# Performance work log

Measured on AMD Instinct MI355X. Metric: run time of the kernel, lower is better.

The kernel has to match this reference:

```python
import jax, jax.numpy as jnp
import numpy as np
from jax import lax

B, N, K, NCP = 4, 2048, 20, 400
EPS = 1e-5


def _bn(x, gamma, beta, axes):
    # training-mode batch norm (biased variance), channel axis = 1
    m = jnp.mean(x, axis=axes, keepdims=True)
    v = jnp.var(x, axis=axes, keepdims=True)
    shape = [1] * x.ndim
    shape[1] = -1
    return (x - m) * lax.rsqrt(v + EPS) * gamma.reshape(shape) + beta.reshape(shape)


def _knn_idx(x, k):
    # x: [B, C, N] -> idx [B, N, k] (nearest, includes self like torch.cdist+topk(largest=False))
    x2 = jnp.sum(x * x, axis=1)  # [B, N]
    d = x2[:, :, None] + x2[:, None, :] - 2.0 * jnp.einsum('bcn,bcm->bnm', x, x)
    return lax.top_k(-d, k)[1]


def _edge_conv(x, w, gamma, beta, k):
    # x: [B, C, N], w: [O, 2C] -> [B, O, N] (1x1 conv + BN + LeakyReLU + max over k)
    idx = _knn_idx(x, k)                      # [B, N, k]
    xt = jnp.transpose(x, (0, 2, 1))          # [B, N, C]
    b = jnp.arange(xt.shape[0])[:, None, None]
    nbr = xt[b, idx]                          # [B, N, k, C]
    ctr = xt[:, :, None, :]
    feat = jnp.concatenate([nbr - ctr, jnp.broadcast_to(ctr, nbr.shape)], axis=-1)  # [B, N, k, 2C]
    y = jnp.einsum('bnkc,oc->bonk', feat, w)  # [B, O, N, k]
    y = jax.nn.leaky_relu(_bn(y, gamma, beta, axes=(0, 2, 3)), 0.2)
    return jnp.max(y, axis=-1)                # [B, O, N]


def setup_inputs() -> dict:
    key = jax.random.key(0)
    ks = jax.random.split(key, 16)
    rnd = lambda k_, s: jax.random.normal(k_, s, dtype=jnp.float32) * 0.02
    inp = {
        'x': jax.random.normal(ks[0], (B, 3, N), dtype=jnp.float32),
        'w1': rnd(ks[1], (64, 6)),    'g1': jnp.ones(64),   'b1': jnp.zeros(64),
        'w2': rnd(ks[2], (128, 128)), 'g2': jnp.ones(128),  'b2': jnp.zeros(128),
        'w3': rnd(ks[3], (256, 256)), 'g3': jnp.ones(256),  'b3': jnp.zeros(256),
        'w4': rnd(ks[4], (512, 512)), 'g4': jnp.ones(512),  'b4': jnp.zeros(512),
        'w5': rnd(ks[5], (2048, 963)), 'g5': jnp.ones(2048), 'b5': jnp.zeros(2048),
        'w6': rnd(ks[6], (2048, 2048)), 'wb6': jnp.zeros(2048), 'g6': jnp.ones(2048), 'b6': jnp.zeros(2048),
        'w7': rnd(ks[7], (4096, 4096)), 'wb7': jnp.zeros(4096), 'g7': jnp.ones(4096), 'b7': jnp.zeros(4096),
        'w8': rnd(ks[8], (NCP, 4096)), 'wb8': jnp.zeros(NCP),
    }
    return inp


def reference(x, w1, g1, b1, w2, g2, b2, w3, g3, b3, w4, g4, b4,
              w5, g5, b5, w6, wb6, g6, b6, w7, wb7, g7, b7, w8, wb8):
    x0 = x                                            # [B, 3, N]
    x1 = _edge_conv(x0, w1, g1, b1, K)                # [B, 64, N]
    x2 = _edge_conv(x1, w2, g2, b2, K)                # [B, 128, N]
    x3 = _edge_conv(x2, w3, g3, b3, K)                # [B, 256, N]
    x4 = _edge_conv(x3, w4, g4, b4, K)                # [B, 512, N]
    h = jnp.concatenate([x0, x1, x2, x3, x4], axis=1) # [B, 963, N]
    h = jnp.einsum('bcn,oc->bon', h, w5)              # [B, 2048, N]
    h = jax.nn.leaky_relu(_bn(h, g5, b5, axes=(0, 2)), 0.2)
    p = jnp.max(h, axis=-1, keepdims=True)            # [B, 2048, 1] global max pool
    y = jnp.einsum('bcl,oc->bol', p, w6) + wb6[None, :, None]
    y = jax.nn.relu(_bn(y, g6, b6, axes=(0, 2)))
    y = jnp.concatenate([y, p], axis=1)               # [B, 4096, 1]
    y = jnp.einsum('bcl,oc->bol', y, w7) + wb7[None, :, None]
    y = jax.nn.relu(_bn(y, g7, b7, axes=(0, 2)))
    y = jnp.einsum('bcl,oc->bol', y, w8) + wb8[None, :, None]
    return jnp.tanh(y[:, :, 0])                       # [B, NCP]
```

## Files before the change

kernel.cpp:

```cpp
#include <hip/hip_runtime.h>
#include <float.h>
#include <math.h>


#define NPTS 2048
#define BATCH 4
#define KNN 20
#define CH_H 963
#define KPAD 992
#define HSTRIDE (CH_H*NPTS)

typedef _Float16 half8 __attribute__((ext_vector_type(8)));
typedef float f32x4 __attribute__((ext_vector_type(4)));

typedef const __attribute__((address_space(1))) unsigned int* gas_p;
typedef __attribute__((address_space(3))) unsigned int* las_p;
__device__ __forceinline__ void gl_lds16(const void* g, void* l){
  __builtin_amdgcn_global_load_lds((gas_p)g, (las_p)l, 16, 0, 0);
}

__device__ __forceinline__ unsigned fenc(float x){
  unsigned u = __float_as_uint(x);
  return (u & 0x80000000u) ? ~u : (u | 0x80000000u);
}
__device__ __forceinline__ float fdec(unsigned u){
  u = (u & 0x80000000u) ? (u ^ 0x80000000u) : ~u;
  return __uint_as_float(u);
}

__global__ void k_convert(const float* __restrict__ x, float* __restrict__ H){
  int i = blockIdx.x*256 + threadIdx.x;
  if (i >= BATCH*3*NPTS) return;
  int b = i / (3*NPTS); int r = i % (3*NPTS);
  H[(size_t)b*HSTRIDE + r] = x[i];
}

__global__ void k_norms(const float* __restrict__ X, int C, float* __restrict__ X2,
                        float* __restrict__ SUMZ){
  int i = blockIdx.x*256 + threadIdx.x;
  if (i < 1024) SUMZ[i] = 0.f;
  int b = i >> 11, n = i & 2047;
  const float* Xb = X + (size_t)b*HSTRIDE + n;
  float s = 0.f;
  for (int c=0;c<C;++c){ float v = Xb[(size_t)c*NPTS]; s = fmaf(v,v,s); }
  X2[i] = s;
}

__global__ __launch_bounds__(256) void k_xsplit(const float* __restrict__ X, int C, int Cpad,
        _Float16* __restrict__ Xhi, _Float16* __restrict__ Xlo)
{
  __shared__ float t[64][65];
  int b = blockIdx.z;
  int n0 = blockIdx.x*64, c0 = blockIdx.y*64;
  int tid = threadIdx.x; int l = tid & 63, m = tid >> 6;
  for (int cc = m; cc < 64; cc += 4){
    int c = c0 + cc;
    t[cc][l] = (c < C) ? X[(size_t)b*HSTRIDE + (size_t)c*NPTS + n0 + l] : 0.f;
  }
  __syncthreads();
  for (int nn = m; nn < 64; nn += 4){
    int c = c0 + l;
    if (c < Cpad){
      float v = t[l][nn];
      _Float16 h = (_Float16)v;
      size_t o = ((size_t)(b<<11)+n0+nn)*Cpad + c;
      Xhi[o] = h;
      Xlo[o] = (_Float16)(v - (float)h);
    }
  }
}

__global__ void k_wsplit(const float* __restrict__ W, int C, int Cpad, int O,
        _Float16* __restrict__ Wh, _Float16* __restrict__ Wl){
  int i = blockIdx.x*256 + threadIdx.x;
  if (i >= 2*O*Cpad) return;
  int op = i / Cpad, c = i - op*Cpad;
  float v = 0.f;
  if (c < C){
    const float* wr = W + (size_t)(op < O ? op : op - O)*(2*C);
    v = (op < O) ? wr[c] : (wr[C+c] - wr[c]);
  }
  _Float16 h = (_Float16)v;
  Wh[i] = h; Wl[i] = (_Float16)(v - (float)h);
}

__global__ __launch_bounds__(256) void k_gram(const _Float16* __restrict__ Xhi,
        const _Float16* __restrict__ Xlo, int Cpad, int bbase,
        float* __restrict__ G0, float* __restrict__ G1)
{
  __shared__ half8 AsH[2][128][4]; __shared__ half8 AsL[2][128][4];
  __shared__ half8 BsH[2][128][4]; __shared__ half8 BsL[2][128][4];
  int bl = blockIdx.z;
  int b  = bbase + bl;
  float* G = bl ? G1 : G0;
  const _Float16* Hb = Xhi + (size_t)(b<<11)*Cpad;
  const _Float16* Lb = Xlo + (size_t)(b<<11)*Cpad;
  int t = blockIdx.x;
  int i = 0, rem = t;
  while (rem >= 16 - i){ rem -= 16 - i; ++i; }
  int j = i + rem;
  int n0 = i*128, m0 = j*128;
  int tid = threadIdx.x;
  int w = tid>>6, lane = tid&63;
  int wm = w>>1, wn = w&1;
  int quad = lane>>4, col = lane&15;
  int wbase = w*128;
  f32x4 acc[4][4];
  #pragma unroll
  for (int a=0;a<4;++a)
    #pragma unroll
    for (int c2=0;c2<4;++c2) acc[a][c2] = (f32x4){0.f,0.f,0.f,0.f};

  auto stageg = [&](int buf, int k0){
    #pragma unroll
    for (int s=0;s<2;++s){
      int cid = wbase + s*64 + lane;
      int row = cid>>2, kc = cid&3;
      size_t ao = (size_t)(n0+row)*Cpad + k0 + kc*8;
      size_t bo = (size_t)(m0+row)*Cpad + k0 + kc*8;
      int lo = (wbase + s*64)*16;
      gl_lds16(Hb + ao, (char*)&AsH[buf][0][0] + lo);
      gl_lds16(Lb + ao, (char*)&AsL[buf][0][0] + lo);
      gl_lds16(Hb + bo, (char*)&BsH[buf][0][0] + lo);
      gl_lds16(Lb + bo, (char*)&BsL[buf][0][0] + lo);
    }
  };

  int NT = Cpad >> 5;
  stageg(0, 0);
  if (NT > 1) stageg(1, 32);
  for (int kt=0; kt<NT; ++kt){
    int buf = kt & 1;
    if (kt+1 < NT) asm volatile("s_waitcnt vmcnt(8)" ::: "memory");
    else           asm volatile("s_waitcnt vmcnt(0)" ::: "memory");
    __builtin_amdgcn_s_barrier();
    __builtin_amdgcn_sched_barrier(0);
    half8 ah[4], al[4], bh[4], blo[4];
    #pragma unroll
    for (int mt=0;mt<4;++mt){ ah[mt] = AsH[buf][wm*64 + mt*16 + col][quad];
                              al[mt] = AsL[buf][wm*64 + mt*16 + col][quad]; }
    #pragma unroll
    for (int nt=0;nt<4;++nt){ bh[nt] = BsH[buf][wn*64 + nt*16 + col][quad];
                              blo[nt] = BsL[buf][wn*64 + nt*16 + col][quad]; }
    #pragma unroll
    for (int mt=0;mt<4;++mt)
      #pragma unroll
      for (int nt=0;nt<4;++nt){
        acc[mt][nt] = __builtin_amdgcn_mfma_f32_16x16x32_f16(ah[mt], bh[nt], acc[mt][nt], 0, 0, 0);
        acc[mt][nt] = __builtin_amdgcn_mfma_f32_16x16x32_f16(ah[mt], blo[nt], acc[mt][nt], 0, 0, 0);
        acc[mt][nt] = __builtin_amdgcn_mfma_f32_16x16x32_f16(al[mt], bh[nt], acc[mt][nt], 0, 0, 0);
      }
    __builtin_amdgcn_sched_barrier(0);
    __builtin_amdgcn_s_barrier();
    if (kt+2 < NT) stageg(buf, (kt+2)<<5);
  }
  bool mirror = (i != j);
  #pragma unroll
  for (int mt=0;mt<4;++mt){
    #pragma unroll
    for (int r=0;r<4;++r){
      int n = n0 + wm*64 + mt*16 + quad*4 + r;
      #pragma unroll
      for (int nt=0;nt<4;++nt){
        int m = m0 + wn*64 + nt*16 + col;
        float y = acc[mt][nt][r];
        G[(size_t)n*2048 + m] = y;
        if (mirror) G[(size_t)m*2048 + n] = y;
      }
    }
  }
}

__global__ __launch_bounds__(256) void k_vu_mfma(const _Float16* __restrict__ Xh,
        const _Float16* __restrict__ Xl, const _Float16* __restrict__ Wh,
        const _Float16* __restrict__ Wl, int Cpad, int O,
        float* __restrict__ V, float* __restrict__ U)
{
  __shared__ half8 AsH[2][128][4]; __shared__ half8 AsL[2][128][4];
  __shared__ half8 BsH[2][128][4]; __shared__ half8 BsL[2][128][4];
  int b = blockIdx.z;
  const _Float16* Hb = Xh + (size_t)(b<<11)*Cpad;
  const _Float16* Lb = Xl + (size_t)(b<<11)*Cpad;
  int n0 = blockIdx.x*128, o0 = blockIdx.y*128;
  int tid = threadIdx.x;
  int w = tid>>6, lane = tid&63;
  int wm = w>>1, wn = w&1;
  int quad = lane>>4, col = lane&15;
  int wbase = w*128;
  f32x4 acc[4][4];
  #pragma unroll
  for (int i=0;i<4;++i)
    #pragma unroll
    for (int j=0;j<4;++j) acc[i][j] = (f32x4){0.f,0.f,0.f,0.f};

  auto stagev = [&](int buf, int k0){
    #pragma unroll
    for (int i=0;i<2;++i){
      int cid = wbase + i*64 + lane;
      int row = cid>>2, kc = cid&3;
      size_t ao = (size_t)(n0+row)*Cpad + k0 + kc*8;
      size_t bo = (size_t)(o0+row)*Cpad + k0 + kc*8;
      int lo = (wbase + i*64)*16;
      gl_lds16(Hb + ao, (char*)&AsH[buf][0][0] + lo);
      gl_lds16(Lb + ao, (char*)&AsL[buf][0][0] + lo);
      gl_lds16(Wh + bo, (char*)&BsH[buf][0][0] + lo);
      gl_lds16(Wl + bo, (char*)&BsL[buf][0][0] + lo);
    }
  };

  int NT = Cpad >> 5;
  stagev(0, 0);
  if (NT > 1) stagev(1, 32);
  for (int kt=0; kt<NT; ++kt){
    int buf = kt & 1;
    if (kt+1 < NT) asm volatile("s_waitcnt vmcnt(8)" ::: "memory");
    else           asm volatile("s_waitcnt vmcnt(0)" ::: "memory");
    __builtin_amdgcn_s_barrier();
    __builtin_amdgcn_sched_barrier(0);
    half8 ah[4], al[4], bh[4], blo[4];
    #pragma unroll
    for (int mt=0;mt<4;++mt){ ah[mt] = AsH[buf][wm*64 + mt*16 + col][quad];
                              al[mt] = AsL[buf][wm*64 + mt*16 + col][quad]; }
    #pragma unroll
    for (int nt=0;nt<4;++nt){ bh[nt] = BsH[buf][wn*64 + nt*16 + col][quad];
                              blo[nt] = BsL[buf][wn*64 + nt*16 + col][quad]; }
    #pragma unroll
    for (int mt=0;mt<4;++mt)
      #pragma unroll
      for (int nt=0;nt<4;++nt){
        acc[mt][nt] = __builtin_amdgcn_mfma_f32_16x16x32_f16(ah[mt], bh[nt], acc[mt][nt], 0, 0, 0);
        acc[mt][nt] = __builtin_amdgcn_mfma_f32_16x16x32_f16(ah[mt], blo[nt], acc[mt][nt], 0, 0, 0);
        acc[mt][nt] = __builtin_amdgcn_mfma_f32_16x16x32_f16(al[mt], bh[nt], acc[mt][nt], 0, 0, 0);
      }
    __builtin_amdgcn_sched_barrier(0);
    __builtin_amdgcn_s_barrier();
    if (kt+2 < NT) stagev(buf, (kt+2)<<5);
  }
  #pragma unroll
  for (int mt=0;mt<4;++mt){
    #pragma unroll
    for (int r=0;r<4;++r){
      int n = n0 + wm*64 + mt*16 + quad*4 + r;
      size_t R = (size_t)(b<<11) + n;
      #pragma unroll
      for (int nt=0;nt<4;++nt){
        int op = o0 + wn*64 + nt*16 + col;
        float y = acc[mt][nt][r];
        if (op < O) V[R*O + op] = y;
        else        U[R*O + op - O] = y;
      }
    }
  }
}

#define KNN_CH(OPC) OPC(0) OPC(1) OPC(2) OPC(3) OPC(4) OPC(5) OPC(6) OPC(7)
#define DECL_CH(ch) float d##ch##_0,d##ch##_1,d##ch##_2,d##ch##_3;
#define LOADG_CH(ch) { float4 g = *(const float4*)(grow + (ch)*256 + base); \
  float4 xm = *(const float4*)(x2b + (ch)*256 + base); \
  d##ch##_0 = x2n + xm.x - 2.f*g.x; d##ch##_1 = x2n + xm.y - 2.f*g.y; \
  d##ch##_2 = x2n + xm.z - 2.f*g.z; d##ch##_3 = x2n + xm.w - 2.f*g.w; }
#define DECL_G(ch) float gv##ch; int gm##ch;
#define MKCH(ch) { gv##ch = d##ch##_0; gm##ch = (ch)*256 + base; \
  if (d##ch##_1 < gv##ch){ gv##ch = d##ch##_1; gm##ch = (ch)*256 + base + 1; } \
  if (d##ch##_2 < gv##ch){ gv##ch = d##ch##_2; gm##ch = (ch)*256 + base + 2; } \
  if (d##ch##_3 < gv##ch){ gv##ch = d##ch##_3; gm##ch = (ch)*256 + base + 3; } }
#define REMCASE(ch) case ch: { \
  if (own){ if (cp==0) d##ch##_0 = FLT_MAX; else if (cp==1) d##ch##_1 = FLT_MAX; \
            else if (cp==2) d##ch##_2 = FLT_MAX; else d##ch##_3 = FLT_MAX; } \
  MKCH(ch) } break;

__global__ __launch_bounds__(256,4) void k_sel(const float* __restrict__ G0,
        const float* __restrict__ G1, const float* __restrict__ X2,
        int bbase, int* __restrict__ IDX)
{
  int tid = threadIdx.x;
  int w = tid >> 6, lane = tid & 63;
  int n = blockIdx.x*4 + w;
  int b = bbase + blockIdx.y;
  const float* grow = (blockIdx.y ? G1 : G0) + (size_t)n*2048;
  const float* x2b  = X2 + (b<<11);
  float x2n = x2b[n];
  int base = lane << 2;
  KNN_CH(DECL_CH)
  KNN_CH(LOADG_CH)
  KNN_CH(DECL_G)
  KNN_CH(MKCH)
  int* op = IDX + ((size_t)(b<<11)+n)*KNN;
  for (int it=0; it<KNN; ++it){
    float v = fminf(fminf(fminf(gv0,gv1),fminf(gv2,gv3)),
                    fminf(fminf(gv4,gv5),fminf(gv6,gv7)));
    #pragma unroll
    for (int s=1; s<64; s<<=1) v = fminf(v, __shfl_xor(v, s));
    int mc = 0x7fffffff;
    mc = (gv7==v) ? gm7 : mc;
    mc = (gv6==v) ? gm6 : mc;
    mc = (gv5==v) ? gm5 : mc;
    mc = (gv4==v) ? gm4 : mc;
    mc = (gv3==v) ? gm3 : mc;
    mc = (gv2==v) ? gm2 : mc;
    mc = (gv1==v) ? gm1 : mc;
    mc = (gv0==v) ? gm0 : mc;
    int m = mc;
    #pragma unroll
    for (int s=1; s<64; s<<=1) m = min(m, __shfl_xor(m, s));
    if (lane==0) op[it] = m;
    int sm = __builtin_amdgcn_readfirstlane(m);
    bool own = (lane == ((sm>>2)&63));
    int cp = sm & 3;
    switch (sm >> 8){ KNN_CH(REMCASE) }
  }
}

template<int OC, int CHN>
__global__ __launch_bounds__(256) void k_gather(const float* __restrict__ V,
        const float* __restrict__ U, const int* __restrict__ IDX,
        float* __restrict__ YMX, float* __restrict__ YMN,
        float* __restrict__ SUM, float* __restrict__ SUMSQ)
{
  constexpr int O = OC*CHN;
  constexpr int NT = 8;
  constexpr int NSTEP = 256/OC;
  __shared__ int sidx[NT*KNN];
  __shared__ float rs[256], rq[256];
  int bid = blockIdx.x;
  int xcd  = bid & 7;
  int b    = xcd >> 1;
  int half = xcd & 1;
  int r    = bid >> 3;
  int ngrp, chunk;
  if (CHN == 1){ ngrp = (half<<7) | r; chunk = 0; }
  else         { ngrp = r & 255; chunk = half*(CHN/2) + (r>>8); }
  int n0 = ngrp * NT;
  int tid = threadIdx.x;
  for (int l = tid; l < NT*KNN; l += 256)
    sidx[l] = IDX[((size_t)(b<<11)+n0)*KNN + l];
  __syncthreads();
  int o  = chunk*OC + (tid & (OC-1));
  int ns = tid / OC;
  const float* Vb = V + (size_t)(b<<11)*O + o;
  float s = 0.f, q = 0.f;
  #pragma unroll
  for (int i = 0; i < NT/NSTEP; ++i){
    int nn = ns + i*NSTEP;
    int n = n0 + nn;
    size_t ub = ((size_t)(b<<11)+n)*O + o;
    float sv = 0.f, sv2 = 0.f, mx = -FLT_MAX, mn = FLT_MAX;
    #pragma unroll
    for (int k=0;k<KNN;++k){
      int m = sidx[nn*KNN+k];
      float v = Vb[(size_t)m*O];
      mx = fmaxf(mx,v); mn = fminf(mn,v);
      sv += v; sv2 = fmaf(v,v,sv2);
    }
    float u = __builtin_nontemporal_load(U + ub);
    __builtin_nontemporal_store(mx + u, YMX + ub);
    __builtin_nontemporal_store(mn + u, YMN + ub);
    s += sv + (float)KNN * u;
    q += sv2 + 2.f*u*sv + (float)KNN*u*u;
  }
  rs[tid] = s; rq[tid] = q;
  __syncthreads();
  if (tid < OC){
    #pragma unroll
    for (int t=1; t<NSTEP; ++t){ s += rs[tid + t*OC]; q += rq[tid + t*OC]; }
    atomicAdd(&SUM[o], s);
    atomicAdd(&SUMSQ[o], q);
  }
}

__global__ void k_finalize(const float* __restrict__ SUM, const float* __restrict__ SUMSQ,
        const float* __restrict__ g, const float* __restrict__ bt,
        int O, float invM, float* __restrict__ SC, float* __restrict__ SH){
  int o = blockIdx.x*256 + threadIdx.x;
  if (o>=O) return;
  float m = SUM[o]*invM;
  float var = SUMSQ[o]*invM - m*m;
  float sc = g[o] * rsqrtf(var + 1e-5f);
  SC[o]=sc; SH[o] = bt[o] - m*sc;
}

__global__ __launch_bounds__(256) void k_apply(const float* __restrict__ YMX, const float* __restrict__ YMN,
        const float* __restrict__ SC, const float* __restrict__ SH,
        int O, float* __restrict__ OUT)
{
  __shared__ float t[64][65];
  int b = blockIdx.z;
  int o0 = blockIdx.y*64, n0 = blockIdx.x*64;
  int tid = threadIdx.x;
  int lo = tid & 63, ln = tid >> 6;
  float sc = SC[o0+lo], sh = SH[o0+lo];
  for (int nn = ln; nn < 64; nn += 4){
    size_t idx = ((size_t)(b<<11)+n0+nn)*O + o0 + lo;
    float v = (sc >= 0.f) ? YMX[idx] : YMN[idx];
    float y = fmaf(sc, v, sh);
    y = (y > 0.f) ? y : 0.2f*y;
    t[lo][nn] = y;
  }
  __syncthreads();
  for (int oo = ln; oo < 64; oo += 4){
    OUT[(size_t)b*HSTRIDE + (size_t)(o0+oo)*NPTS + n0 + lo] = t[oo][lo];
  }
}

__global__ __launch_bounds__(256) void k_h2f16(const float* __restrict__ H, _Float16* __restrict__ Hf){
  __shared__ float t[64][65];
  int b = blockIdx.z;
  int n0 = blockIdx.x*64, c0 = blockIdx.y*64;
  int tid = threadIdx.x; int l = tid & 63, m = tid >> 6;
  for (int cc = m; cc < 64; cc += 4){
    int c = c0 + cc;
    t[cc][l] = (c < CH_H) ? H[(size_t)b*HSTRIDE + (size_t)c*NPTS + n0 + l] : 0.f;
  }
  __syncthreads();
  for (int nn = m; nn < 64; nn += 4){
    int c = c0 + l;
    if (c < KPAD)
      Hf[((size_t)(b<<11)+n0+nn)*KPAD + c] = (_Float16)t[l][nn];
  }
}

__global__ void k_w5f16(const float* __restrict__ w5, _Float16* __restrict__ Wf,
                        unsigned* __restrict__ z){
  int i = blockIdx.x*256 + threadIdx.x;
  if (i < 12288) z[i] = 0u;
  else if (i < 20480) z[i] = 0xFFFFFFFFu;
  if (i >= 2048*KPAD) return;
  int o = i / KPAD, c = i - o*KPAD;
  Wf[i] = (c < CH_H) ? (_Float16)w5[(size_t)o*CH_H + c] : (_Float16)0.f;
}

__global__ __launch_bounds__(256) void k_l5mfma(const _Float16* __restrict__ Wf,
        const _Float16* __restrict__ Hf,
        float* __restrict__ SUM5, float* __restrict__ SUMSQ5,
        unsigned* __restrict__ MAXB, unsigned* __restrict__ MINB)
{
  __shared__ half8 As[2][128][4];
  __shared__ half8 Bs[2][128][4];
  int b  = blockIdx.z;
  int n0 = blockIdx.x*128, o0 = blockIdx.y*128;
  int tid = threadIdx.x;
  int w = tid>>6, lane = tid&63;
  int wm = w>>1, wn = w&1;
  int quad = lane>>4, col = lane&15;
  int wbase = w*128;
  f32x4 acc[4][4];
  #pragma unroll
  for (int i=0;i<4;++i)
    #pragma unroll
    for (int j=0;j<4;++j) acc[i][j] = (f32x4){0.f,0.f,0.f,0.f};

  auto stage5 = [&](int buf, int k0){
    #pragma unroll
    for (int i=0;i<2;++i){
      int cid = wbase + i*64 + lane;
      int row = cid>>2, kc = cid&3;
      int lo = (wbase + i*64)*16;
      gl_lds16(Wf + (size_t)(o0+row)*KPAD + k0 + kc*8, (char*)&As[buf][0][0] + lo);
      gl_lds16(Hf + ((size_t)(b<<11)+n0+row)*KPAD + k0 + kc*8, (char*)&Bs[buf][0][0] + lo);
    }
  };

  const int NT = KPAD/32;
  stage5(0, 0);
  stage5(1, 32);
  for (int kt=0; kt<NT; ++kt){
    int buf = kt & 1;
    if (kt+1 < NT) asm volatile("s_waitcnt vmcnt(4)" ::: "memory");
    else           asm volatile("s_waitcnt vmcnt(0)" ::: "memory");
    __builtin_amdgcn_s_barrier();
    __builtin_amdgcn_sched_barrier(0);
    half8 af[4], bf[4];
    #pragma unroll
    for (int mt=0;mt<4;++mt) af[mt] = As[buf][wm*64 + mt*16 + col][quad];
    #pragma unroll
    for (int nt=0;nt<4;++nt) bf[nt] = Bs[buf][wn*64 + nt*16 + col][quad];
    #pragma unroll
    for (int mt=0;mt<4;++mt)
      #pragma unroll
      for (int nt=0;nt<4;++nt)
        acc[mt][nt] = __builtin_amdgcn_mfma_f32_16x16x32_f16(af[mt], bf[nt], acc[mt][nt], 0, 0, 0);
    __builtin_amdgcn_sched_barrier(0);
    __builtin_amdgcn_s_barrier();
    if (kt+2 < NT) stage5(buf, (kt+2)*32);
  }
  #pragma unroll
  for (int mt=0;mt<4;++mt){
    #pragma unroll
    for (int r=0;r<4;++r){
      float s=0.f, q=0.f, mx=-FLT_MAX, mn=FLT_MAX;
      #pragma unroll
      for (int nt=0;nt<4;++nt){
        float y = acc[mt][nt][r];
        s += y; q = fmaf(y,y,q);
        mx = fmaxf(mx,y); mn = fminf(mn,y);
      }
      #pragma unroll
      for (int d=8; d; d>>=1){
        s += __shfl_down(s,(unsigned)d,16);
        q += __shfl_down(q,(unsigned)d,16);
        mx = fmaxf(mx,__shfl_down(mx,(unsigned)d,16));
        mn = fminf(mn,__shfl_down(mn,(unsigned)d,16));
      }
      if (col==0){
        int o = o0 + wm*64 + mt*16 + quad*4 + r;
        atomicAdd(&SUM5[o], s);
        atomicAdd(&SUMSQ5[o], q);
        atomicMax(&MAXB[(b<<11)+o], fenc(mx));
        atomicMin(&MINB[(b<<11)+o], fenc(mn));
      }
    }
  }
}

__global__ void k_l5_final(const float* __restrict__ SUM5, const float* __restrict__ SUMSQ5,
        const unsigned* __restrict__ MAXB, const unsigned* __restrict__ MINB,
        const float* __restrict__ g5, const float* __restrict__ b5, float* __restrict__ P)
{
  int o = blockIdx.x*256 + threadIdx.x;
  if (o>=2048) return;
  float m = SUM5[o]*(1.f/8192.f);
  float var = SUMSQ5[o]*(1.f/8192.f) - m*m;
  float sc = g5[o] * rsqrtf(var + 1e-5f);
  float sh = b5[o] - m*sc;
  for (int b=0;b<4;++b){
    float mx = fdec(MAXB[b*2048+o]);
    float mn = fdec(MINB[b*2048+o]);
    float v = (sc >= 0.f) ? fmaf(sc,mx,sh) : fmaf(sc,mn,sh);
    v = (v > 0.f) ? v : 0.2f*v;
    P[b*2048 + o] = v;
  }
}

__global__ __launch_bounds__(256) void k_fc(const float* __restrict__ W, const float* __restrict__ bias,
        const float* __restrict__ Z, int Cin, int O, float* __restrict__ Y)
{
  int o = blockIdx.x*4 + (threadIdx.x>>6);
  int lane = threadIdx.x & 63;
  if (o >= O) return;
  const float* wr = W + (size_t)o*Cin;
  float a0=0.f,a1=0.f,a2=0.f,a3=0.f;
  for (int c=lane;c<Cin;c+=64){
    float w = wr[c];
    a0 = fmaf(w, Z[c],        a0);
    a1 = fmaf(w, Z[Cin+c],    a1);
    a2 = fmaf(w, Z[2*Cin+c],  a2);
    a3 = fmaf(w, Z[3*Cin+c],  a3);
  }
  #pragma unroll
  for (int s=32;s;s>>=1){
    a0 += __shfl_down(a0,(unsigned)s); a1 += __shfl_down(a1,(unsigned)s);
    a2 += __shfl_down(a2,(unsigned)s); a3 += __shfl_down(a3,(unsigned)s);
  }
  if (lane==0){
    float bb = bias[o];
    Y[o]=a0+bb; Y[O+o]=a1+bb; Y[2*O+o]=a2+bb; Y[3*O+o]=a3+bb;
  }
}

__global__ void k_bn4(const float* __restrict__ Y, const float* __restrict__ g, const float* __restrict__ bt,
                      int O, float* __restrict__ Z, int zstride, int zoff)
{
  int o = blockIdx.x*256 + threadIdx.x;
  if (o>=O) return;
  float v0=Y[o], v1=Y[O+o], v2=Y[2*O+o], v3=Y[3*O+o];
  float m = 0.25f*(v0+v1+v2+v3);
  float d0=v0-m, d1=v1-m, d2=v2-m, d3=v3-m;
  float var = 0.25f*(d0*d0+d1*d1+d2*d2+d3*d3);
  float sc = g[o] * rsqrtf(var + 1e-5f);
  float sh = bt[o] - m*sc;
  Z[0*zstride+zoff+o] = fmaxf(fmaf(sc,v0,sh), 0.f);
  Z[1*zstride+zoff+o] = fmaxf(fmaf(sc,v1,sh), 0.f);
  Z[2*zstride+zoff+o] = fmaxf(fmaf(sc,v2,sh), 0.f);
  Z[3*zstride+zoff+o] = fmaxf(fmaf(sc,v3,sh), 0.f);
}

__global__ void k_copy_p(const float* __restrict__ P, float* __restrict__ Z){
  int i = blockIdx.x*256 + threadIdx.x;
  int b = i>>11, o = i&2047;
  Z[b*4096 + 2048 + o] = P[i];
}

__global__ __launch_bounds__(256) void k_final(const float* __restrict__ W8, const float* __restrict__ wb8,
        const float* __restrict__ Z7, float* __restrict__ out)
{
  int o = blockIdx.x*4 + (threadIdx.x>>6);
  int lane = threadIdx.x & 63;
  if (o >= 400) return;
  const float* wr = W8 + (size_t)o*4096;
  float a0=0.f,a1=0.f,a2=0.f,a3=0.f;
  for (int c=lane;c<4096;c+=64){
    float w = wr[c];
    a0 = fmaf(w, Z7[c],        a0);
    a1 = fmaf(w, Z7[4096+c],   a1);
    a2 = fmaf(w, Z7[2*4096+c], a2);
    a3 = fmaf(w, Z7[3*4096+c], a3);
  }
  #pragma unroll
  for (int s=32;s;s>>=1){
    a0 += __shfl_down(a0,(unsigned)s); a1 += __shfl_down(a1,(unsigned)s);
    a2 += __shfl_down(a2,(unsigned)s); a3 += __shfl_down(a3,(unsigned)s);
  }
  if (lane==0){
    float bb = wb8[o];
    out[0*400+o] = tanhf(a0+bb);
    out[1*400+o] = tanhf(a1+bb);
    out[2*400+o] = tanhf(a2+bb);
    out[3*400+o] = tanhf(a3+bb);
  }
}

extern "C" void kernel_launch(void* const* d_in, const int* in_sizes, int n_in,
                              void* d_out, int out_size, void* d_ws, size_t ws_size,
                              hipStream_t stream)
{
  const float* x   = (const float*)d_in[0];
  const float* w_e[4]  = {(const float*)d_in[1], (const float*)d_in[4], (const float*)d_in[7], (const float*)d_in[10]};
  const float* g_e[4]  = {(const float*)d_in[2], (const float*)d_in[5], (const float*)d_in[8], (const float*)d_in[11]};
  const float* b_e[4]  = {(const float*)d_in[3], (const float*)d_in[6], (const float*)d_in[9], (const float*)d_in[12]};
  const float* w5  = (const float*)d_in[13];
  const float* g5  = (const float*)d_in[14];
  const float* b5  = (const float*)d_in[15];
  const float* w6  = (const float*)d_in[16];
  const float* wb6 = (const float*)d_in[17];
  const float* g6  = (const float*)d_in[18];
  const float* b6  = (const float*)d_in[19];
  const float* w7  = (const float*)d_in[20];
  const float* wb7 = (const float*)d_in[21];
  const float* g7  = (const float*)d_in[22];
  const float* b7  = (const float*)d_in[23];
  const float* w8  = (const float*)d_in[24];
  const float* wb8 = (const float*)d_in[25];

  float* WS = (float*)d_ws;
  float* H    = WS;
  float* V    = WS + 7888896;
  float* U    = V  + 4194304;
  float* YMX  = U  + 4194304;
  float* YMN  = YMX+ 4194304;
  int*   IDX  = (int*)(YMN + 4194304);
  float* X2   = (float*)(IDX + 163840);
  float* SUM  = X2 + 8192;
  float* SUMSQ= SUM + 512;
  float* SC   = SUMSQ + 512;
  float* SH   = SC + 512;
  float* SUM5 = SH + 512;
  float* SUMSQ5 = SUM5 + 2048;
  unsigned* MAXB = (unsigned*)(SUMSQ5 + 2048);
  unsigned* MINB = MAXB + 8192;
  float* P    = (float*)(MINB + 8192);
  float* Y6   = P + 8192;
  float* Z    = Y6 + 8192;
  float* Y7   = Z + 16384;
  float* Z7   = Y7 + 16384;
  _Float16* Hf  = (_Float16*)V;
  _Float16* Wf  = (_Float16*)U;
  _Float16* Xhi  = (_Float16*)YMN;
  _Float16* Xlo  = Xhi + (size_t)4*2048*256;
  _Float16* Wsph = Xlo + (size_t)4*2048*256;
  _Float16* Wspl = Wsph + 1024*256;
  float* G0 = YMX;
  float* G1 = V;

  k_convert<<<96,256,0,stream>>>(x, H);

  const int Cin_[4]  = {3,64,128,256};
  const int Cpad_[4] = {32,64,128,256};
  const int O_[4]    = {64,128,256,512};
  const int ioff_[4] = {0,3,67,195};
  const int ooff_[4] = {3,67,195,451};

  for (int l=0;l<4;++l){
    const float* Xl = H + (size_t)ioff_[l]*NPTS;
    int C = Cin_[l], Cpad = Cpad_[l], O = O_[l];
    k_norms<<<32,256,0,stream>>>(Xl, C, X2, SUM);
    dim3 gxs(32, (Cpad+63)/64, 4);
    k_xsplit<<<gxs,256,0,stream>>>(Xl, C, Cpad, Xhi, Xlo);
    k_wsplit<<<(2*O*Cpad+255)/256,256,0,stream>>>(w_e[l], C, Cpad, O, Wsph, Wspl);
    dim3 ggr(136,1,2);
    k_gram<<<ggr,256,0,stream>>>(Xhi, Xlo, Cpad, 0, G0, G1);
    dim3 gsl(512,2);
    k_sel<<<gsl,256,0,stream>>>(G0, G1, X2, 0, IDX);
    k_gram<<<ggr,256,0,stream>>>(Xhi, Xlo, Cpad, 2, G0, G1);
    k_sel<<<gsl,256,0,stream>>>(G0, G1, X2, 2, IDX);
    dim3 gvm(16, (2*O)/128, 4);
    k_vu_mfma<<<gvm,256,0,stream>>>(Xhi, Xlo, Wsph, Wspl, Cpad, O, V, U);
    if (O == 64)
      k_gather<64,1><<<1024,256,0,stream>>>(V, U, IDX, YMX, YMN, SUM, SUMSQ);
    else if (O == 128)
      k_gather<128,1><<<1024,256,0,stream>>>(V, U, IDX, YMX, YMN, SUM, SUMSQ);
    else if (O == 256)
      k_gather<128,2><<<2048,256,0,stream>>>(V, U, IDX, YMX, YMN, SUM, SUMSQ);
    else
      k_gather<128,4><<<4096,256,0,stream>>>(V, U, IDX, YMX, YMN, SUM, SUMSQ);
    k_finalize<<<2,256,0,stream>>>(SUM, SUMSQ, g_e[l], b_e[l], O, 1.f/163840.f, SC, SH);
    dim3 gap(32, O/64, 4);
    k_apply<<<gap,256,0,stream>>>(YMX, YMN, SC, SH, O, H + (size_t)ooff_[l]*NPTS);
  }

  dim3 gtr(32,16,4);
  k_h2f16<<<gtr,256,0,stream>>>(H, Hf);
  k_w5f16<<<(2048*KPAD+255)/256,256,0,stream>>>(w5, Wf, (unsigned*)SUM5);
  dim3 g5g(16,16,4);
  k_l5mfma<<<g5g,256,0,stream>>>(Wf, Hf, SUM5, SUMSQ5, MAXB, MINB);
  k_l5_final<<<8,256,0,stream>>>(SUM5, SUMSQ5, MAXB, MINB, g5, b5, P);

  k_fc<<<512,256,0,stream>>>(w6, wb6, P, 2048, 2048, Y6);
  k_bn4<<<8,256,0,stream>>>(Y6, g6, b6, 2048, Z, 4096, 0);
  k_copy_p<<<32,256,0,stream>>>(P, Z);
  k_fc<<<1024,256,0,stream>>>(w7, wb7, Z, 4096, 4096, Y7);
  k_bn4<<<16,256,0,stream>>>(Y7, g7, b7, 4096, Z7, 4096, 0);
  k_final<<<100,256,0,stream>>>(w8, wb8, Z7, (float*)d_out);
}
```

Measured before the change: 1.102 ms.

## Remap GEMM workgroups across XCDs and compute full Gram matrix without mirroring

```diff
diff --git a/kernel.cpp b/kernel.cpp
--- a/kernel.cpp
+++ b/kernel.cpp
@@ -90,16 +90,16 @@
 {
   __shared__ half8 AsH[2][128][4]; __shared__ half8 AsL[2][128][4];
   __shared__ half8 BsH[2][128][4]; __shared__ half8 BsL[2][128][4];
-  int bl = blockIdx.z;
+  int wg = blockIdx.x;
+  int id2 = (wg & 7)*64 + (wg >> 3);
+  int bl = id2 >> 8;
+  int j  = (id2 >> 4) & 15;
+  int i  = id2 & 15;
   int b  = bbase + bl;
   float* G = bl ? G1 : G0;
   const _Float16* Hb = Xhi + (size_t)(b<<11)*Cpad;
   const _Float16* Lb = Xlo + (size_t)(b<<11)*Cpad;
-  int t = blockIdx.x;
-  int i = 0, rem = t;
-  while (rem >= 16 - i){ rem -= 16 - i; ++i; }
-  int j = i + rem;
-  int n0 = i*128, m0 = j*128;
+  int m0 = i*128, n0 = j*128;
   int tid = threadIdx.x;
   int w = tid>>6, lane = tid&63;
   int wm = w>>1, wn = w&1;
@@ -154,7 +154,6 @@
     __builtin_amdgcn_s_barrier();
     if (kt+2 < NT) stageg(buf, (kt+2)<<5);
   }
-  bool mirror = (i != j);
   #pragma unroll
   for (int mt=0;mt<4;++mt){
     #pragma unroll
@@ -163,9 +162,7 @@
       #pragma unroll
       for (int nt=0;nt<4;++nt){
         int m = m0 + wn*64 + nt*16 + col;
-        float y = acc[mt][nt][r];
-        G[(size_t)n*2048 + m] = y;
-        if (mirror) G[(size_t)m*2048 + n] = y;
+        G[(size_t)n*2048 + m] = acc[mt][nt][r];
       }
     }
   }
@@ -178,10 +175,15 @@
 {
   __shared__ half8 AsH[2][128][4]; __shared__ half8 AsL[2][128][4];
   __shared__ half8 BsH[2][128][4]; __shared__ half8 BsL[2][128][4];
-  int b = blockIdx.z;
+  int wg = blockIdx.x;
+  int NY = gridDim.x >> 6;
+  int id2 = (wg & 7)*(NY<<3) + (wg >> 3);
+  int o_t = id2 >> 6;
+  int b   = (id2 >> 4) & 3;
+  int n_t = id2 & 15;
   const _Float16* Hb = Xh + (size_t)(b<<11)*Cpad;
   const _Float16* Lb = Xl + (size_t)(b<<11)*Cpad;
-  int n0 = blockIdx.x*128, o0 = blockIdx.y*128;
+  int n0 = n_t*128, o0 = o_t*128;
   int tid = threadIdx.x;
   int w = tid>>6, lane = tid&63;
   int wm = w>>1, wn = w&1;
@@ -436,8 +438,12 @@
 {
   __shared__ half8 As[2][128][4];
   __shared__ half8 Bs[2][128][4];
-  int b  = blockIdx.z;
-  int n0 = blockIdx.x*128, o0 = blockIdx.y*128;
+  int wg = blockIdx.x;
+  int id2 = (wg & 7)*128 + (wg >> 3);
+  int o_t = id2 >> 6;
+  int b   = (id2 >> 4) & 3;
+  int n_t = id2 & 15;
+  int n0 = n_t*128, o0 = o_t*128;
   int tid = threadIdx.x;
   int w = tid>>6, lane = tid&63;
   int wm = w>>1, wn = w&1;
@@ -676,14 +682,12 @@
     dim3 gxs(32, (Cpad+63)/64, 4);
     k_xsplit<<<gxs,256,0,stream>>>(Xl, C, Cpad, Xhi, Xlo);
     k_wsplit<<<(2*O*Cpad+255)/256,256,0,stream>>>(w_e[l], C, Cpad, O, Wsph, Wspl);
-    dim3 ggr(136,1,2);
-    k_gram<<<ggr,256,0,stream>>>(Xhi, Xlo, Cpad, 0, G0, G1);
+    k_gram<<<512,256,0,stream>>>(Xhi, Xlo, Cpad, 0, G0, G1);
     dim3 gsl(512,2);
     k_sel<<<gsl,256,0,stream>>>(G0, G1, X2, 0, IDX);
-    k_gram<<<ggr,256,0,stream>>>(Xhi, Xlo, Cpad, 2, G0, G1);
+    k_gram<<<512,256,0,stream>>>(Xhi, Xlo, Cpad, 2, G0, G1);
     k_sel<<<gsl,256,0,stream>>>(G0, G1, X2, 2, IDX);
-    dim3 gvm(16, (2*O)/128, 4);
-    k_vu_mfma<<<gvm,256,0,stream>>>(Xhi, Xlo, Wsph, Wspl, Cpad, O, V, U);
+    k_vu_mfma<<<64*(2*O/128),256,0,stream>>>(Xhi, Xlo, Wsph, Wspl, Cpad, O, V, U);
     if (O == 64)
       k_gather<64,1><<<1024,256,0,stream>>>(V, U, IDX, YMX, YMN, SUM, SUMSQ);
     else if (O == 128)
@@ -700,8 +704,7 @@
   dim3 gtr(32,16,4);
   k_h2f16<<<gtr,256,0,stream>>>(H, Hf);
   k_w5f16<<<(2048*KPAD+255)/256,256,0,stream>>>(w5, Wf, (unsigned*)SUM5);
-  dim3 g5g(16,16,4);
-  k_l5mfma<<<g5g,256,0,stream>>>(Wf, Hf, SUM5, SUMSQ5, MAXB, MINB);
+  k_l5mfma<<<1024,256,0,stream>>>(Wf, Hf, SUM5, SUMSQ5, MAXB, MINB);
   k_l5_final<<<8,256,0,stream>>>(SUM5, SUMSQ5, MAXB, MINB, g5, b5, P);
 
   k_fc<<<512,256,0,stream>>>(w6, wb6, P, 2048, 2048, Y6);
```

Result: faster. 1.026 ms (-6.9%).
